# Kernel tuning notes

Measured on AMD Instinct MI355X. Metric: run time of the kernel, lower is better.

## Reference

```python
import jax, jax.numpy as jnp
import numpy as np

EMBED = 1024
HEAD = 64
SEQ = 2048
BATCH = 8


def setup_inputs() -> dict:
    key = jax.random.key(0)
    kx, kq, kk, kv = jax.random.split(key, 4)
    x = jax.random.normal(kx, (BATCH, SEQ, EMBED), dtype=jnp.float32)
    # torch nn.Linear weight is [out,in]; we store [in,out] so y = x @ W
    Wq = jax.random.normal(kq, (EMBED, HEAD), dtype=jnp.float32) * (EMBED ** -0.5)
    Wk = jax.random.normal(kk, (EMBED, HEAD), dtype=jnp.float32) * (EMBED ** -0.5)
    Wv = jax.random.normal(kv, (EMBED, HEAD), dtype=jnp.float32) * (EMBED ** -0.5)
    return {"x": x, "Wq": Wq, "Wk": Wk, "Wv": Wv}


def reference(x, Wq, Wk, Wv):
    # x: [B,T,C]; single-head causal attention. Scale uses C (embedding dim),
    # matching the original module's C ** (-0.5). Dropout in eval mode (identity).
    B, T, C = x.shape
    q = x @ Wq  # [B,T,H]
    k = x @ Wk  # [B,T,H]
    v = x @ Wv  # [B,T,H]
    scores = jnp.einsum('bqh,bkh->bqk', q, k) * (C ** -0.5)  # [B,T,T]
    causal = jnp.tril(jnp.ones((T, T), dtype=bool))
    scores = jnp.where(causal, scores, -jnp.inf)
    weights = jax.nn.softmax(scores, axis=-1)
    return jnp.einsum('bqk,bkh->bqh', weights, v)  # [B,T,H]
```

## Files before the change

### kernel.cpp

```cpp
#include <hip/hip_runtime.h>
#include <hip/hip_bf16.h>
#include <math.h>

#define BATCH 8
#define SEQ 2048
#define EMBED 1024
#define HEAD 64
#define NROWS (BATCH*SEQ)

typedef short bf16x8 __attribute__((ext_vector_type(8)));
typedef short bf16x4 __attribute__((ext_vector_type(4)));
typedef float f32x4  __attribute__((ext_vector_type(4)));

__device__ inline short f2bf(float f) {
    __hip_bfloat16 h = __float2bfloat16(f);
    return *(short*)&h;
}
__device__ inline float bf2f(short s) {
    __hip_bfloat16 h = *(__hip_bfloat16*)&s;
    return __bfloat162float(h);
}

#define NSLOT 144
__device__ __host__ inline int triOff(int qt) {
    int g = qt >> 2;
    return 2 * g * (g + 1) + (qt & 3) * (g + 1);
}

__global__ __launch_bounds__(256) void prep_w(
    const float* __restrict__ Wq, const float* __restrict__ Wk,
    const float* __restrict__ Wv, short* __restrict__ wt)
{
    int g    = blockIdx.x * 256 + threadIdx.x;
    int lane = g & 63;
    int frag = g >> 6;
    int k32  = frag & 31;
    int ct   = frag >> 5;
    int col  = ct * 16 + (lane & 15);
    int mm   = col >> 6, cc = col & 63;
    const float* W = (mm == 0) ? Wq : ((mm == 1) ? Wk : Wv);
    int kb = k32 * 32 + (lane >> 4) * 8;
    bf16x8 o;
#pragma unroll
    for (int j = 0; j < 8; j++)
        o[j] = f2bf(W[(size_t)(kb + j) * HEAD + cc]);
    *(bf16x8*)&wt[(size_t)g * 8] = o;
}

__global__ __launch_bounds__(512, 4) void proj_kernel(
    const float* __restrict__ x, const short* __restrict__ wt,
    short* __restrict__ q, short* __restrict__ k, short* __restrict__ vt)
{
    __shared__ short xs[32][1024];
    float* psum = (float*)&xs[0][0];

    const int tid  = threadIdx.x;
    const int wave = tid >> 6, lane = tid & 63;
    const int m16  = lane & 15, quad = lane >> 4;
    const int cg   = wave & 3;
    const int kh   = wave >> 2;
    const int r0   = blockIdx.x * 32;

    {
        const int row  = tid >> 4;
        const int col4 = tid & 15;
        const float* xr = x + (size_t)(r0 + row) * EMBED;
#pragma unroll
        for (int h = 0; h < 2; h++) {
            float4 f[8];
#pragma unroll
            for (int i = 0; i < 8; i++)
                f[i] = *(const float4*)&xr[(h * 8 + i) * 64 + col4 * 4];
#pragma unroll
            for (int i = 0; i < 8; i++) {
                int c  = (h * 8 + i) * 64 + col4 * 4;
                int k8 = c >> 3, rem = c & 7;
                int cs = ((k8 ^ (row & 7)) << 3) + rem;
                bf16x4 bv;
                bv[0] = f2bf(f[i].x); bv[1] = f2bf(f[i].y);
                bv[2] = f2bf(f[i].z); bv[3] = f2bf(f[i].w);
                *(bf16x4*)&xs[row][cs] = bv;
            }
        }
    }
    __syncthreads();

    f32x4 acc[2][3];
#pragma unroll
    for (int mt = 0; mt < 2; mt++)
#pragma unroll
        for (int j = 0; j < 3; j++) acc[mt][j] = (f32x4){0.f, 0.f, 0.f, 0.f};

#pragma unroll 4
    for (int s = 0; s < 16; s++) {
        int k32  = kh * 16 + s;
        int ksw  = ((k32 * 4 + quad) ^ (m16 & 7)) << 3;
        bf16x8 a0 = *(const bf16x8*)&xs[m16][ksw];
        bf16x8 a1 = *(const bf16x8*)&xs[16 + m16][ksw];
#pragma unroll
        for (int j = 0; j < 3; j++) {
            int ct = cg * 3 + j;
            bf16x8 bb = *(const bf16x8*)&wt[(size_t)((ct * 32 + k32) * 64 + lane) * 8];
            acc[0][j] = __builtin_amdgcn_mfma_f32_16x16x32_bf16(a0, bb, acc[0][j], 0, 0, 0);
            acc[1][j] = __builtin_amdgcn_mfma_f32_16x16x32_bf16(a1, bb, acc[1][j], 0, 0, 0);
        }
    }

    __syncthreads();
    if (kh == 1) {
        float* p = psum + ((size_t)(cg * 64 + lane) * 24);
#pragma unroll
        for (int mt = 0; mt < 2; mt++)
#pragma unroll
            for (int j = 0; j < 3; j++)
                *(f32x4*)&p[(mt * 3 + j) * 4] = acc[mt][j];
    }
    __syncthreads();
    if (kh == 0) {
        const float* p = psum + ((size_t)(cg * 64 + lane) * 24);
        const int bb = r0 >> 11;
        const int tb = r0 & 2047;
#pragma unroll
        for (int mt = 0; mt < 2; mt++)
#pragma unroll
            for (int j = 0; j < 3; j++) {
                f32x4 o = acc[mt][j] + *(const f32x4*)&p[(mt * 3 + j) * 4];
                int gcol = (cg * 3 + j) * 16 + m16;
                int mm = gcol >> 6, cc = gcol & 63;
                if (mm < 2) {
                    short* op = (mm == 0) ? q : k;
#pragma unroll
                    for (int reg = 0; reg < 4; reg++) {
                        int row = r0 + mt * 16 + quad * 4 + reg;
                        op[(size_t)row * HEAD + cc] = f2bf(o[reg]);
                    }
                } else {
                    bf16x4 pk;
                    pk[0] = f2bf(o[0]); pk[1] = f2bf(o[1]);
                    pk[2] = f2bf(o[2]); pk[3] = f2bf(o[3]);
                    int t = tb + mt * 16 + quad * 4;
                    *(bf16x4*)&vt[(((size_t)bb * 64 + cc) << 11) + t] = pk;
                }
            }
    }
}

__global__ __launch_bounds__(256, 2) void attn_kernel(
    const short* __restrict__ qg, const short* __restrict__ kg,
    const short* __restrict__ vtg,
    short* __restrict__ pO, float* __restrict__ pl)
{
    __shared__ short ksh[256][72];
    __shared__ short vsh[64][264];
    __shared__ short psh[4][16][72];

    const int qt  = blockIdx.x;
    const int seg = blockIdx.y;
    const int b   = blockIdx.z;
    const int c0  = seg * 4;
    const int c1  = min(c0 + 4, qt + 1);
    if (c0 >= c1) return;
    const int nch = c1 - c0;

    const int tid  = threadIdx.x;
    const int wave = tid >> 6, lane = tid & 63;
    const int m16  = lane & 15, quad = lane >> 4;
    const float scale = 0.03125f;

    const short* qb  = qg  + (size_t)b * SEQ * HEAD;
    const short* kb  = kg  + (size_t)b * SEQ * HEAD;
    const short* vtb = vtg + (size_t)b * HEAD * SEQ;

    bf16x8 a_q0, a_q1;
    {
        const int qrow = qt * 64 + wave * 16 + m16;
        a_q0 = *(const bf16x8*)&qb[(size_t)qrow * HEAD + quad * 8];
        a_q1 = *(const bf16x8*)&qb[(size_t)qrow * HEAD + 32 + quad * 8];
    }

    {
        const int kt  = tid >> 2;
        const int kh8 = (tid & 3) * 16;
#pragma unroll
        for (int cc = 0; cc < 4; cc++) {
            const int t0 = (c0 + cc) * 64;
            bf16x8 k0 = *(const bf16x8*)&kb[(size_t)(t0 + kt) * HEAD + kh8];
            bf16x8 k1 = *(const bf16x8*)&kb[(size_t)(t0 + kt) * HEAD + kh8 + 8];
            *(bf16x8*)&ksh[cc * 64 + kt][kh8]     = k0;
            *(bf16x8*)&ksh[cc * 64 + kt][kh8 + 8] = k1;
            bf16x8 v0 = *(const bf16x8*)&vtb[((size_t)kt << 11) + t0 + kh8];
            bf16x8 v1 = *(const bf16x8*)&vtb[((size_t)kt << 11) + t0 + kh8 + 8];
            *(bf16x8*)&vsh[kt][cc * 64 + kh8]     = v0;
            *(bf16x8*)&vsh[kt][cc * 64 + kh8 + 8] = v1;
        }
    }
    __syncthreads();

    f32x4 o_acc[4];
#pragma unroll
    for (int i = 0; i < 4; i++) o_acc[i] = (f32x4){0.f, 0.f, 0.f, 0.f};
    float lsum[4] = {0.f, 0.f, 0.f, 0.f};

    for (int cc = 0; cc < nch; cc++) {
        const int c  = c0 + cc;
        const int t0 = c * 64;

        f32x4 s_t[4];
#pragma unroll
        for (int nt = 0; nt < 4; nt++) {
            bf16x8 bk0 = *(const bf16x8*)&ksh[cc * 64 + nt * 16 + m16][quad * 8];
            bf16x8 bk1 = *(const bf16x8*)&ksh[cc * 64 + nt * 16 + m16][32 + quad * 8];
            f32x4 acc = (f32x4){0.f, 0.f, 0.f, 0.f};
            acc = __builtin_amdgcn_mfma_f32_16x16x32_bf16(a_q0, bk0, acc, 0, 0, 0);
            acc = __builtin_amdgcn_mfma_f32_16x16x32_bf16(a_q1, bk1, acc, 0, 0, 0);
            s_t[nt] = acc;
        }

        if (c == qt) {
#pragma unroll
            for (int r = 0; r < 4; r++) {
                const int row = qt * 64 + wave * 16 + quad * 4 + r;
#pragma unroll
                for (int nt = 0; nt < 4; nt++) {
                    int tt = t0 + nt * 16 + m16;
                    float p = (tt <= row) ? __expf(s_t[nt][r] * scale) : 0.f;
                    lsum[r] += p;
                    psh[wave][quad * 4 + r][nt * 16 + m16] = f2bf(p);
                }
            }
        } else {
#pragma unroll
            for (int r = 0; r < 4; r++) {
#pragma unroll
                for (int nt = 0; nt < 4; nt++) {
                    float p = __expf(s_t[nt][r] * scale);
                    lsum[r] += p;
                    psh[wave][quad * 4 + r][nt * 16 + m16] = f2bf(p);
                }
            }
        }

#pragma unroll
        for (int ss = 0; ss < 2; ss++) {
            bf16x8 a_p = *(const bf16x8*)&psh[wave][m16][ss * 32 + quad * 8];
#pragma unroll
            for (int ht = 0; ht < 4; ht++) {
                bf16x8 b_v = *(const bf16x8*)&vsh[ht * 16 + m16][cc * 64 + ss * 32 + quad * 8];
                o_acc[ht] = __builtin_amdgcn_mfma_f32_16x16x32_bf16(a_p, b_v, o_acc[ht], 0, 0, 0);
            }
        }
    }

#pragma unroll
    for (int r = 0; r < 4; r++) {
#pragma unroll
        for (int off = 8; off >= 1; off >>= 1)
            lsum[r] += __shfl_xor(lsum[r], off, 64);
    }
    const size_t slot  = (size_t)b * NSLOT + triOff(qt) + seg;
    const size_t pbase = slot * 64;
#pragma unroll
    for (int ht = 0; ht < 4; ht++) {
#pragma unroll
        for (int r = 0; r < 4; r++) {
            int rowt = wave * 16 + quad * 4 + r;
            pO[(pbase + rowt) * 64 + ht * 16 + m16] = f2bf(o_acc[ht][r]);
        }
    }
    if (m16 == 0) {
#pragma unroll
        for (int r = 0; r < 4; r++) {
            int rowt = wave * 16 + quad * 4 + r;
            pl[pbase + rowt] = lsum[r];
        }
    }
}

__global__ __launch_bounds__(256) void combine_kernel(
    const short* __restrict__ pO, const float* __restrict__ pl,
    float* __restrict__ out)
{
    int g   = blockIdx.x * 256 + threadIdx.x;
    int h4  = (g & 15) * 4;
    int row = (g >> 4) & 2047;
    int b   = g >> 15;
    int qt  = row >> 6, lr = row & 63;
    int ns  = (qt >> 2) + 1;
    size_t base = (size_t)b * NSLOT + triOff(qt);
    float4 O = {0.f, 0.f, 0.f, 0.f};
    float  L = 0.f;
    for (int s = 0; s < ns; s++) {
        bf16x4 ov = *(const bf16x4*)&pO[((base + s) * 64 + lr) * 64 + h4];
        O.x += bf2f(ov[0]); O.y += bf2f(ov[1]);
        O.z += bf2f(ov[2]); O.w += bf2f(ov[3]);
        L += pl[(base + s) * 64 + lr];
    }
    float inv = 1.f / L;
    O.x *= inv; O.y *= inv; O.z *= inv; O.w *= inv;
    *(float4*)&out[(size_t)g * 4] = O;
}

extern "C" void kernel_launch(void* const* d_in, const int* in_sizes, int n_in,
                              void* d_out, int out_size, void* d_ws, size_t ws_size,
                              hipStream_t stream) {
    const float* x  = (const float*)d_in[0];
    const float* Wq = (const float*)d_in[1];
    const float* Wk = (const float*)d_in[2];
    const float* Wv = (const float*)d_in[3];
    float* out = (float*)d_out;

    short* q  = (short*)d_ws;
    short* k  = q + (size_t)NROWS * HEAD;
    short* vt = k + (size_t)NROWS * HEAD;
    short* wt = vt + (size_t)NROWS * HEAD;
    short* pO = wt + 196608;
    float* pl = (float*)(pO + (size_t)BATCH * NSLOT * 64 * 64);

    prep_w<<<96, 256, 0, stream>>>(Wq, Wk, Wv, wt);
    proj_kernel<<<512, 512, 0, stream>>>(x, wt, q, k, vt);
    attn_kernel<<<dim3(32, 8, 8), 256, 0, stream>>>(q, k, vt, pO, pl);
    combine_kernel<<<1024, 256, 0, stream>>>(pO, pl, out);
}
```

Measured before the change: 133.2 us.

## Stream K/V chunks through small shared tiles with register prefetch

```diff
diff --git a/kernel.cpp b/kernel.cpp
--- a/kernel.cpp
+++ b/kernel.cpp
@@ -145,22 +145,21 @@
     }
 }
 
-__global__ __launch_bounds__(256, 2) void attn_kernel(
+__global__ __launch_bounds__(256, 5) void attn_kernel(
     const short* __restrict__ qg, const short* __restrict__ kg,
     const short* __restrict__ vtg,
     short* __restrict__ pO, float* __restrict__ pl)
 {
-    __shared__ short ksh[256][72];
-    __shared__ short vsh[64][264];
+    __shared__ short ksh[64][72];
+    __shared__ short vsh[64][72];
     __shared__ short psh[4][16][72];
 
     const int qt  = blockIdx.x;
     const int seg = blockIdx.y;
     const int b   = blockIdx.z;
     const int c0  = seg * 4;
-    const int c1  = min(c0 + 4, qt + 1);
+    const int c1  = min(seg * 4 + 4, qt + 1);
     if (c0 >= c1) return;
-    const int nch = c1 - c0;
 
     const int tid  = threadIdx.x;
     const int wave = tid >> 6, lane = tid & 63;
@@ -178,38 +177,40 @@
         a_q1 = *(const bf16x8*)&qb[(size_t)qrow * HEAD + 32 + quad * 8];
     }
 
-    {
-        const int kt  = tid >> 2;
-        const int kh8 = (tid & 3) * 16;
-#pragma unroll
-        for (int cc = 0; cc < 4; cc++) {
-            const int t0 = (c0 + cc) * 64;
-            bf16x8 k0 = *(const bf16x8*)&kb[(size_t)(t0 + kt) * HEAD + kh8];
-            bf16x8 k1 = *(const bf16x8*)&kb[(size_t)(t0 + kt) * HEAD + kh8 + 8];
-            *(bf16x8*)&ksh[cc * 64 + kt][kh8]     = k0;
-            *(bf16x8*)&ksh[cc * 64 + kt][kh8 + 8] = k1;
-            bf16x8 v0 = *(const bf16x8*)&vtb[((size_t)kt << 11) + t0 + kh8];
-            bf16x8 v1 = *(const bf16x8*)&vtb[((size_t)kt << 11) + t0 + kh8 + 8];
-            *(bf16x8*)&vsh[kt][cc * 64 + kh8]     = v0;
-            *(bf16x8*)&vsh[kt][cc * 64 + kh8 + 8] = v1;
-        }
-    }
-    __syncthreads();
-
     f32x4 o_acc[4];
 #pragma unroll
     for (int i = 0; i < 4; i++) o_acc[i] = (f32x4){0.f, 0.f, 0.f, 0.f};
     float lsum[4] = {0.f, 0.f, 0.f, 0.f};
 
-    for (int cc = 0; cc < nch; cc++) {
-        const int c  = c0 + cc;
+    const int srow = tid >> 3;
+    const int sc8  = (tid & 7) * 8;
+
+    bf16x8 kr0 = *(const bf16x8*)&kb[(size_t)(c0 * 64 + srow) * HEAD + sc8];
+    bf16x8 kr1 = *(const bf16x8*)&kb[(size_t)(c0 * 64 + 32 + srow) * HEAD + sc8];
+    bf16x8 vr0 = *(const bf16x8*)&vtb[((size_t)srow << 11) + c0 * 64 + sc8];
+    bf16x8 vr1 = *(const bf16x8*)&vtb[((size_t)(srow + 32) << 11) + c0 * 64 + sc8];
+
+    for (int c = c0; c < c1; c++) {
         const int t0 = c * 64;
+        __syncthreads();
+        *(bf16x8*)&ksh[srow][sc8]      = kr0;
+        *(bf16x8*)&ksh[srow + 32][sc8] = kr1;
+        *(bf16x8*)&vsh[srow][sc8]      = vr0;
+        *(bf16x8*)&vsh[srow + 32][sc8] = vr1;
+        __syncthreads();
+        if (c + 1 < c1) {
+            const int tn = (c + 1) * 64;
+            kr0 = *(const bf16x8*)&kb[(size_t)(tn + srow) * HEAD + sc8];
+            kr1 = *(const bf16x8*)&kb[(size_t)(tn + 32 + srow) * HEAD + sc8];
+            vr0 = *(const bf16x8*)&vtb[((size_t)srow << 11) + tn + sc8];
+            vr1 = *(const bf16x8*)&vtb[((size_t)(srow + 32) << 11) + tn + sc8];
+        }
 
         f32x4 s_t[4];
 #pragma unroll
         for (int nt = 0; nt < 4; nt++) {
-            bf16x8 bk0 = *(const bf16x8*)&ksh[cc * 64 + nt * 16 + m16][quad * 8];
-            bf16x8 bk1 = *(const bf16x8*)&ksh[cc * 64 + nt * 16 + m16][32 + quad * 8];
+            bf16x8 bk0 = *(const bf16x8*)&ksh[nt * 16 + m16][quad * 8];
+            bf16x8 bk1 = *(const bf16x8*)&ksh[nt * 16 + m16][32 + quad * 8];
             f32x4 acc = (f32x4){0.f, 0.f, 0.f, 0.f};
             acc = __builtin_amdgcn_mfma_f32_16x16x32_bf16(a_q0, bk0, acc, 0, 0, 0);
             acc = __builtin_amdgcn_mfma_f32_16x16x32_bf16(a_q1, bk1, acc, 0, 0, 0);
@@ -245,7 +246,7 @@
             bf16x8 a_p = *(const bf16x8*)&psh[wave][m16][ss * 32 + quad * 8];
 #pragma unroll
             for (int ht = 0; ht < 4; ht++) {
-                bf16x8 b_v = *(const bf16x8*)&vsh[ht * 16 + m16][cc * 64 + ss * 32 + quad * 8];
+                bf16x8 b_v = *(const bf16x8*)&vsh[ht * 16 + m16][ss * 32 + quad * 8];
                 o_acc[ht] = __builtin_amdgcn_mfma_f32_16x16x32_bf16(a_p, b_v, o_acc[ht], 0, 0, 0);
             }
         }
```

Result: faster. 128.4 us (-3.6%).
